# Kernel optimization log

Measured on AMD Instinct MI355X. Metric: run time of the kernel, lower is better.

## Reference

```python
import jax, jax.numpy as jnp
import numpy as np

N_NODES = 50000
N_EDGES = 600000
IN_FEATS = 128
N_HIDDEN = 128
N_CLASSES = 40


def setup_inputs() -> dict:
    key = jax.random.key(0)
    ks = jax.random.split(key, 12)
    feat = jax.random.normal(ks[0], (N_NODES, IN_FEATS), dtype=jnp.float32)
    src = jax.random.randint(ks[1], (N_EDGES,), 0, N_NODES, dtype=jnp.int32)
    dst = jax.random.randint(ks[2], (N_EDGES,), 0, N_NODES, dtype=jnp.int32)
    dims = [(IN_FEATS, N_HIDDEN), (N_HIDDEN, N_HIDDEN), (N_HIDDEN, N_CLASSES)]
    params = {}
    for i, (di, do) in enumerate(dims):
        s = 1.0 / np.sqrt(di)
        params[f"w_self{i}"] = jax.random.uniform(ks[3 + 3 * i], (di, do), jnp.float32, -s, s)
        params[f"w_neigh{i}"] = jax.random.uniform(ks[4 + 3 * i], (di, do), jnp.float32, -s, s)
        params[f"b{i}"] = jnp.zeros((do,), jnp.float32)
    return dict(feat=feat, src=src, dst=dst, **params)


def _sage_layer(h, src, dst, w_self, w_neigh, b):
    # mean aggregation over in-neighbors: msg = h[src], reduce at dst
    msg_sum = jax.ops.segment_sum(h[src], dst, num_segments=N_NODES)  # [N, d]
    deg = jax.ops.segment_sum(jnp.ones((src.shape[0],), h.dtype), dst, num_segments=N_NODES)
    h_neigh = msg_sum / jnp.maximum(deg, 1.0)[:, None]
    # DGL SAGEConv(mean): out = fc_self(h) + fc_neigh(mean_neigh) + bias
    return h @ w_self + h_neigh @ w_neigh + b


def reference(feat, src, dst,
              w_self0, w_neigh0, b0,
              w_self1, w_neigh1, b1,
              w_self2, w_neigh2, b2):
    # dropout p=0.0 -> identity
    h = _sage_layer(feat, src, dst, w_self0, w_neigh0, b0)
    h = jax.nn.relu(h)
    h = _sage_layer(h, src, dst, w_self1, w_neigh1, b1)
    h = jax.nn.relu(h)
    h = _sage_layer(h, src, dst, w_self2, w_neigh2, b2)
    return h
```

## Files before the change

### kernel.cpp

```cpp
#include <hip/hip_runtime.h>

#define N_NODES 50000
#define N_EDGES 600000

typedef short bf16x8 __attribute__((ext_vector_type(8)));
typedef float f32x4  __attribute__((ext_vector_type(4)));
typedef unsigned short u16x8 __attribute__((ext_vector_type(8)));
typedef unsigned short u16x4 __attribute__((ext_vector_type(4)));

__device__ inline ushort rne_bf16(float a) {
    union { float f; unsigned u; } v; v.f = a;
    return (ushort)((v.u + 0x7FFFu + ((v.u >> 16) & 1u)) >> 16);
}
__device__ inline float bf16_to_f32(ushort h) {
    return __uint_as_float((unsigned)h << 16);
}
__device__ inline void split_bf16(float a, ushort& hi, ushort& lo) {
    hi = rne_bf16(a);
    float hv = bf16_to_f32(hi);
    lo = rne_bf16(a - hv);
}


__global__ void count_deg_kernel(const int* __restrict__ dst, int* __restrict__ deg, int ne) {
    int e = blockIdx.x * blockDim.x + threadIdx.x;
    if (e < ne) atomicAdd(&deg[dst[e]], 1);
}

__global__ __launch_bounds__(256) void block_sums_kernel(const int* __restrict__ deg,
                                                         int* __restrict__ bsum, int n) {
    __shared__ int s[256];
    int t = threadIdx.x;
    int i = blockIdx.x * 256 + t;
    s[t] = (i < n) ? deg[i] : 0;
    __syncthreads();
    #pragma unroll
    for (int d = 128; d > 0; d >>= 1) {
        if (t < d) s[t] += s[t + d];
        __syncthreads();
    }
    if (t == 0) bsum[blockIdx.x] = s[0];
}

__global__ __launch_bounds__(256) void scatter_fused_kernel(const int* __restrict__ deg,
                                                            const int* __restrict__ bsum,
                                                            int* __restrict__ off,
                                                            int* __restrict__ cur,
                                                            int n, int nb) {
    __shared__ int s[256];
    int t = threadIdx.x;

    int bv = (t < nb) ? bsum[t] : 0;
    s[t] = bv;
    __syncthreads();
    #pragma unroll
    for (int d = 1; d < 256; d <<= 1) {
        int x = (t >= d) ? s[t - d] : 0;
        __syncthreads();
        s[t] += x;
        __syncthreads();
    }
    int base = (blockIdx.x > 0) ? s[blockIdx.x - 1] : 0;
    if (blockIdx.x == 0 && t == 0) off[n] = s[255];
    __syncthreads();

    int i = blockIdx.x * 256 + t;
    int v = (i < n) ? deg[i] : 0;
    s[t] = v;
    __syncthreads();
    #pragma unroll
    for (int d = 1; d < 256; d <<= 1) {
        int x = (t >= d) ? s[t - d] : 0;
        __syncthreads();
        s[t] += x;
        __syncthreads();
    }
    if (i < n) {
        int excl = s[t] - v + base;
        off[i] = excl;
        cur[i] = excl;
    }
}

__global__ void fill_csr_kernel(const int* __restrict__ src, const int* __restrict__ dst,
                                int* __restrict__ cur, int* __restrict__ ssrc, int ne) {
    int e = blockIdx.x * blockDim.x + threadIdx.x;
    if (e < ne) {
        int p = atomicAdd(&cur[dst[e]], 1);
        ssrc[p] = src[e];
    }
}

__global__ void convert_all_w(const float* __restrict__ ws0, const float* __restrict__ wn0,
                              const float* __restrict__ ws1, const float* __restrict__ wn1,
                              const float* __restrict__ ws2, const float* __restrict__ wn2,
                              ushort* __restrict__ Bth0, ushort* __restrict__ Btl0,
                              ushort* __restrict__ Bth1, ushort* __restrict__ Btl1,
                              ushort* __restrict__ Bth2, ushort* __restrict__ Btl2) {
    int b = blockIdx.x;
    int k = threadIdx.x;
    const float *Ws, *Wn;
    ushort *H, *L;
    int dout, n;
    if (b < 256)      { n = b;       dout = 128; Ws = ws0; Wn = wn0; H = Bth0; L = Btl0; }
    else if (b < 512) { n = b - 256; dout = 128; Ws = ws1; Wn = wn1; H = Bth1; L = Btl1; }
    else              { n = b - 512; dout = 40;  Ws = ws2; Wn = wn2; H = Bth2; L = Btl2; }
    float w = (n < dout) ? Ws[(long)k * dout + n] : Wn[(long)k * dout + (n - dout)];
    ushort hi, lo;
    split_bf16(w, hi, lo);
    H[n * 128 + k] = hi;
    L[n * 128 + k] = lo;
}


#define KDIM 128
#define APAD 136

__device__ inline void stage_a32(const float* __restrict__ A, int bm, int M, int tid,
                                 ushort* __restrict__ Ahi, ushort* __restrict__ Alo) {
    const int m   = tid >> 3;
    const int seg = (tid & 7) * 16;
    const int grow = bm + m;
    float f[16];
    if (grow < M) {
        const float* ap = A + (long)grow * KDIM + seg;
        #pragma unroll
        for (int q = 0; q < 4; ++q) {
            float4 a = *(const float4*)(ap + q * 4);
            f[q * 4 + 0] = a.x; f[q * 4 + 1] = a.y;
            f[q * 4 + 2] = a.z; f[q * 4 + 3] = a.w;
        }
    } else {
        #pragma unroll
        for (int i = 0; i < 16; ++i) f[i] = 0.f;
    }
    ushort h[16], l[16];
    #pragma unroll
    for (int i = 0; i < 16; ++i) split_bf16(f[i], h[i], l[i]);
    #pragma unroll
    for (int q = 0; q < 2; ++q) {
        uint4 hw, lw;
        hw.x = (unsigned)h[q*8+0] | ((unsigned)h[q*8+1] << 16);
        hw.y = (unsigned)h[q*8+2] | ((unsigned)h[q*8+3] << 16);
        hw.z = (unsigned)h[q*8+4] | ((unsigned)h[q*8+5] << 16);
        hw.w = (unsigned)h[q*8+6] | ((unsigned)h[q*8+7] << 16);
        lw.x = (unsigned)l[q*8+0] | ((unsigned)l[q*8+1] << 16);
        lw.y = (unsigned)l[q*8+2] | ((unsigned)l[q*8+3] << 16);
        lw.z = (unsigned)l[q*8+4] | ((unsigned)l[q*8+5] << 16);
        lw.w = (unsigned)l[q*8+6] | ((unsigned)l[q*8+7] << 16);
        *(uint4*)&Ahi[m * APAD + seg + q * 8] = hw;
        *(uint4*)&Alo[m * APAD + seg + q * 8] = lw;
    }
}

__global__ __launch_bounds__(256, 4) void gemm_mfma_wide(
    const float* __restrict__ A,
    const ushort* __restrict__ Bth, const ushort* __restrict__ Btl,
    const float* __restrict__ bias,
    float* __restrict__ S, ushort* __restrict__ T, int M)
{
    __shared__ ushort Ahi[32 * APAD];
    __shared__ ushort Alo[32 * APAD];

    const int tid = threadIdx.x;
    const int wave = tid >> 6;
    const int lane = tid & 63;
    const int lane16 = lane & 15;
    const int quad = lane >> 4;
    const int bm = blockIdx.x * 32;
    const int colbase = wave * 64;

    stage_a32(A, bm, M, tid, Ahi, Alo);
    __syncthreads();

    f32x4 acc[2][4] = {};

    #pragma unroll
    for (int c = 0; c < 4; ++c) {
        const int k0 = c * 32 + quad * 8;
        bf16x8 ah[2], al[2];
        #pragma unroll
        for (int r = 0; r < 2; ++r) {
            int off = (16 * r + lane16) * APAD + k0;
            ah[r] = *(const bf16x8*)&Ahi[off];
            al[r] = *(const bf16x8*)&Alo[off];
        }
        #pragma unroll
        for (int ct = 0; ct < 4; ++ct) {
            const long boff = (long)(colbase + 16 * ct + lane16) * KDIM + k0;
            bf16x8 bh = *(const bf16x8*)(Bth + boff);
            bf16x8 bl = *(const bf16x8*)(Btl + boff);
            #pragma unroll
            for (int r = 0; r < 2; ++r) {
                acc[r][ct] = __builtin_amdgcn_mfma_f32_16x16x32_bf16(bh, ah[r], acc[r][ct], 0, 0, 0);
                acc[r][ct] = __builtin_amdgcn_mfma_f32_16x16x32_bf16(bl, ah[r], acc[r][ct], 0, 0, 0);
                acc[r][ct] = __builtin_amdgcn_mfma_f32_16x16x32_bf16(bh, al[r], acc[r][ct], 0, 0, 0);
            }
        }
    }

    #pragma unroll
    for (int ct = 0; ct < 4; ++ct) {
        const int col0 = colbase + 16 * ct + quad * 4;
        const bool toS = col0 < 128;
        f32x4 bv = {0,0,0,0};
        if (toS) bv = *(const f32x4*)(bias + col0);
        #pragma unroll
        for (int r = 0; r < 2; ++r) {
            const int row = bm + 16 * r + lane16;
            if (row < M) {
                if (toS) {
                    *(f32x4*)(S + (long)row * 128 + col0) = acc[r][ct] + bv;
                } else {
                    u16x4 t4;
                    #pragma unroll
                    for (int i = 0; i < 4; ++i) t4[i] = rne_bf16(acc[r][ct][i]);
                    *(u16x4*)(T + (long)row * 128 + (col0 - 128)) = t4;
                }
            }
        }
    }
}

__global__ __launch_bounds__(256, 4) void gemm_mfma_narrow(
    const float* __restrict__ A,
    const ushort* __restrict__ Bth, const ushort* __restrict__ Btl,
    const float* __restrict__ bias,
    float* __restrict__ S, ushort* __restrict__ T, int M)
{
    __shared__ ushort Ahi[32 * APAD];
    __shared__ ushort Alo[32 * APAD];

    const int tid = threadIdx.x;
    const int wave = tid >> 6;
    const int lane = tid & 63;
    const int lane16 = lane & 15;
    const int quad = lane >> 4;
    const int bm = blockIdx.x * 32;

    const int rt = wave & 1;
    const int cg = wave >> 1;
    const int ctbase = cg * 3;
    const int nct = cg ? 2 : 3;

    stage_a32(A, bm, M, tid, Ahi, Alo);
    __syncthreads();

    f32x4 acc[3] = {};

    #pragma unroll
    for (int c = 0; c < 4; ++c) {
        const int off = (rt * 16 + lane16) * APAD + c * 32 + quad * 8;
        bf16x8 ah = *(const bf16x8*)&Ahi[off];
        bf16x8 al = *(const bf16x8*)&Alo[off];
        #pragma unroll
        for (int j = 0; j < 3; ++j) {
            if (j < nct) {
                const int ct = ctbase + j;
                const long boff = (long)(16 * ct + lane16) * KDIM + c * 32 + quad * 8;
                bf16x8 bh = *(const bf16x8*)(Bth + boff);
                bf16x8 bl = *(const bf16x8*)(Btl + boff);
                acc[j] = __builtin_amdgcn_mfma_f32_16x16x32_bf16(bh, ah, acc[j], 0, 0, 0);
                acc[j] = __builtin_amdgcn_mfma_f32_16x16x32_bf16(bl, ah, acc[j], 0, 0, 0);
                acc[j] = __builtin_amdgcn_mfma_f32_16x16x32_bf16(bh, al, acc[j], 0, 0, 0);
            }
        }
    }

    #pragma unroll
    for (int j = 0; j < 3; ++j) {
        if (j < nct) {
            const int ct = ctbase + j;
            const int col0 = 16 * ct + quad * 4;
            const bool toS = col0 < 40;
            const int row = bm + rt * 16 + lane16;
            if (row < M) {
                if (toS) {
                    f32x4 bv = *(const f32x4*)(bias + col0);
                    *(f32x4*)(S + (long)row * 40 + col0) = acc[j] + bv;
                } else {
                    u16x4 t4;
                    #pragma unroll
                    for (int i = 0; i < 4; ++i) t4[i] = rne_bf16(acc[j][i]);
                    *(u16x4*)(T + (long)row * 40 + (col0 - 40)) = t4;
                }
            }
        }
    }
}


template <int RELU>
__global__ __launch_bounds__(256) void agg128_kernel(
    const float* __restrict__ S, const ushort* __restrict__ T,
    const int* __restrict__ off, const int* __restrict__ ssrc,
    float* __restrict__ out, int nnodes)
{
    const int node = (blockIdx.x * 256 + threadIdx.x) >> 6;
    if (node >= nnodes) return;
    const int lane = threadIdx.x & 63;
    const int slot = lane >> 4;
    const int col8 = (lane & 15) * 8;

    const int a = off[node];
    const int b = off[node + 1];

    f32x4 acc0a = {0,0,0,0}, acc0b = {0,0,0,0};
    f32x4 acc1a = {0,0,0,0}, acc1b = {0,0,0,0};

    int i = a;
    for (; i + 8 <= b; i += 8) {
        int s0 = ssrc[i + slot];
        int s1 = ssrc[i + 4 + slot];
        u16x8 v0 = *(const u16x8*)(T + (long)s0 * 128 + col8);
        u16x8 v1 = *(const u16x8*)(T + (long)s1 * 128 + col8);
        #pragma unroll
        for (int j = 0; j < 4; ++j) {
            acc0a[j] += bf16_to_f32(v0[j]);
            acc0b[j] += bf16_to_f32(v0[4 + j]);
            acc1a[j] += bf16_to_f32(v1[j]);
            acc1b[j] += bf16_to_f32(v1[4 + j]);
        }
    }
    for (; i < b; i += 4) {
        int e = i + slot;
        if (e < b) {
            int s = ssrc[e];
            u16x8 v = *(const u16x8*)(T + (long)s * 128 + col8);
            #pragma unroll
            for (int j = 0; j < 4; ++j) {
                acc0a[j] += bf16_to_f32(v[j]);
                acc0b[j] += bf16_to_f32(v[4 + j]);
            }
        }
    }
    f32x4 accA = acc0a + acc1a;
    f32x4 accB = acc0b + acc1b;

    #pragma unroll
    for (int m = 16; m <= 32; m <<= 1) {
        #pragma unroll
        for (int j = 0; j < 4; ++j) {
            accA[j] += __shfl_xor((float)accA[j], m);
            accB[j] += __shfl_xor((float)accB[j], m);
        }
    }

    if (slot == 0) {
        int deg = b - a;
        float scale = (deg > 0) ? (1.0f / (float)deg) : 0.f;
        f32x4 sA = *(const f32x4*)(S + (long)node * 128 + col8);
        f32x4 sB = *(const f32x4*)(S + (long)node * 128 + col8 + 4);
        f32x4 rA = sA + accA * scale;
        f32x4 rB = sB + accB * scale;
        if (RELU) {
            #pragma unroll
            for (int j = 0; j < 4; ++j) {
                rA[j] = fmaxf(rA[j], 0.f);
                rB[j] = fmaxf(rB[j], 0.f);
            }
        }
        *(f32x4*)(out + (long)node * 128 + col8) = rA;
        *(f32x4*)(out + (long)node * 128 + col8 + 4) = rB;
    }
}

template <int RELU>
__global__ __launch_bounds__(256) void agg40_kernel(
    const float* __restrict__ S, const ushort* __restrict__ T,
    const int* __restrict__ off, const int* __restrict__ ssrc,
    float* __restrict__ out, int nnodes)
{
    const int node = (blockIdx.x * 256 + threadIdx.x) >> 6;
    if (node >= nnodes) return;
    const int lane = threadIdx.x & 63;
    const bool active = lane < 60;
    const int slot = active ? (lane / 10) : 5;
    const int fi = lane % 10;
    const int fo = fi * 4;

    const int a = off[node];
    const int b = off[node + 1];

    f32x4 acc0 = {0,0,0,0}, acc1 = {0,0,0,0};

    int i = a;
    for (; i + 12 <= b; i += 12) {
        int s0 = ssrc[i + slot];
        int s1 = ssrc[i + 6 + slot];
        u16x4 v0 = *(const u16x4*)(T + (long)s0 * 40 + fo);
        u16x4 v1 = *(const u16x4*)(T + (long)s1 * 40 + fo);
        if (active) {
            #pragma unroll
            for (int j = 0; j < 4; ++j) {
                acc0[j] += bf16_to_f32(v0[j]);
                acc1[j] += bf16_to_f32(v1[j]);
            }
        }
    }
    for (; i < b; i += 6) {
        int e = i + slot;
        if (active && e < b) {
            int s = ssrc[e];
            u16x4 v = *(const u16x4*)(T + (long)s * 40 + fo);
            #pragma unroll
            for (int j = 0; j < 4; ++j) acc0[j] += bf16_to_f32(v[j]);
        }
    }
    f32x4 acc = acc0 + acc1;

    f32x4 tot = acc;
    #pragma unroll
    for (int d = 10; d <= 50; d += 10) {
        int srcl = fi + d;
        #pragma unroll
        for (int j = 0; j < 4; ++j) tot[j] += __shfl((float)acc[j], srcl);
    }

    if (lane < 10) {
        int deg = b - a;
        float scale = (deg > 0) ? (1.0f / (float)deg) : 0.f;
        f32x4 s4 = *(const f32x4*)(S + (long)node * 40 + fo);
        f32x4 r = s4 + tot * scale;
        if (RELU) {
            #pragma unroll
            for (int j = 0; j < 4; ++j) r[j] = fmaxf(r[j], 0.f);
        }
        *(f32x4*)(out + (long)node * 40 + fo) = r;
    }
}


extern "C" void kernel_launch(void* const* d_in, const int* in_sizes, int n_in,
                              void* d_out, int out_size, void* d_ws, size_t ws_size,
                              hipStream_t stream) {
    const float* feat = (const float*)d_in[0];
    const int*   src  = (const int*)d_in[1];
    const int*   dst  = (const int*)d_in[2];
    const float* ws0  = (const float*)d_in[3];
    const float* wn0  = (const float*)d_in[4];
    const float* b0   = (const float*)d_in[5];
    const float* ws1  = (const float*)d_in[6];
    const float* wn1  = (const float*)d_in[7];
    const float* b1   = (const float*)d_in[8];
    const float* ws2  = (const float*)d_in[9];
    const float* wn2  = (const float*)d_in[10];
    const float* b2   = (const float*)d_in[11];

    const int N = N_NODES;
    const int NE = N_EDGES;
    const int NB = (N + 255) / 256;

    char* ws = (char*)d_ws;
    int*    offsets = (int*)(ws + 0);
    int*    cursor  = (int*)(ws + 200704);
    int*    degi    = (int*)(ws + 401408);
    int*    bsum    = (int*)(ws + 601600);
    int*    ssrc    = (int*)(ws + 603648);
    ushort* Bth0 = (ushort*)(ws + 200704);
    ushort* Btl0 = (ushort*)(ws + 266240);
    ushort* Bth1 = (ushort*)(ws + 331776);
    ushort* Btl1 = (ushort*)(ws + 397312);
    ushort* Bth2 = (ushort*)(ws + 462848);
    ushort* Btl2 = (ushort*)(ws + 483328);
    float*  hbuf = (float*)(ws + 3003904);
    float*  sbuf = (float*)(ws + 28603904);
    ushort* tbuf = (ushort*)(ws + 54203904);

    hipMemsetAsync(degi, 0, (size_t)N * sizeof(int), stream);
    count_deg_kernel<<<(NE + 255) / 256, 256, 0, stream>>>(dst, degi, NE);
    block_sums_kernel<<<NB, 256, 0, stream>>>(degi, bsum, N);
    scatter_fused_kernel<<<NB, 256, 0, stream>>>(degi, bsum, offsets, cursor, N, NB);
    fill_csr_kernel<<<(NE + 255) / 256, 256, 0, stream>>>(src, dst, cursor, ssrc, NE);

    convert_all_w<<<592, 128, 0, stream>>>(ws0, wn0, ws1, wn1, ws2, wn2,
                                           Bth0, Btl0, Bth1, Btl1, Bth2, Btl2);

    const int gx = (N + 31) / 32;
    const int ga = (N + 3) / 4;

    gemm_mfma_wide<<<gx, 256, 0, stream>>>(feat, Bth0, Btl0, b0, sbuf, tbuf, N);
    agg128_kernel<1><<<ga, 256, 0, stream>>>(sbuf, tbuf, offsets, ssrc, hbuf, N);

    gemm_mfma_wide<<<gx, 256, 0, stream>>>(hbuf, Bth1, Btl1, b1, sbuf, tbuf, N);
    agg128_kernel<1><<<ga, 256, 0, stream>>>(sbuf, tbuf, offsets, ssrc, hbuf, N);

    gemm_mfma_narrow<<<gx, 256, 0, stream>>>(hbuf, Bth2, Btl2, b2, sbuf, tbuf, N);
    agg40_kernel<0><<<ga, 256, 0, stream>>>(sbuf, tbuf, offsets, ssrc, (float*)d_out, N);
}
```

Before: 335.2 us.

## Split wide GEMM columns across block pairs with register-resident B fragments

Each wide-GEMM block now computes only one 128-column half (self or neighbor projection), preloading its B fragments into registers before a grid-stride loop over 32-row tiles. The grid is doubled so each block handles one tile. This halves per-block MFMA work and removes repeated B global loads inside the k-loop, at the cost of staging and splitting each A tile twice and a lower occupancy hint.

```diff
diff --git a/kernel.cpp b/kernel.cpp
--- a/kernel.cpp
+++ b/kernel.cpp
@@ -153,7 +153,7 @@
     }
 }
 
-__global__ __launch_bounds__(256, 4) void gemm_mfma_wide(
+__global__ __launch_bounds__(256, 3) void gemm_mfma_wide(
     const float* __restrict__ A,
     const ushort* __restrict__ Bth, const ushort* __restrict__ Btl,
     const float* __restrict__ bias,
@@ -167,55 +167,66 @@
     const int lane = tid & 63;
     const int lane16 = lane & 15;
     const int quad = lane >> 4;
-    const int bm = blockIdx.x * 32;
-    const int colbase = wave * 64;
-
-    stage_a32(A, bm, M, tid, Ahi, Alo);
-    __syncthreads();
-
-    f32x4 acc[2][4] = {};
-
+    const int half = blockIdx.x & 1;
+    const int colbase = half * 128 + wave * 32;
+    const int ntiles = (M + 31) >> 5;
+
+    bf16x8 Bh[4][2], Bl[4][2];
     #pragma unroll
     for (int c = 0; c < 4; ++c) {
-        const int k0 = c * 32 + quad * 8;
-        bf16x8 ah[2], al[2];
-        #pragma unroll
-        for (int r = 0; r < 2; ++r) {
-            int off = (16 * r + lane16) * APAD + k0;
-            ah[r] = *(const bf16x8*)&Ahi[off];
-            al[r] = *(const bf16x8*)&Alo[off];
-        }
-        #pragma unroll
-        for (int ct = 0; ct < 4; ++ct) {
-            const long boff = (long)(colbase + 16 * ct + lane16) * KDIM + k0;
-            bf16x8 bh = *(const bf16x8*)(Bth + boff);
-            bf16x8 bl = *(const bf16x8*)(Btl + boff);
+        #pragma unroll
+        for (int ct = 0; ct < 2; ++ct) {
+            const long boff = (long)(colbase + 16 * ct + lane16) * KDIM + c * 32 + quad * 8;
+            Bh[c][ct] = *(const bf16x8*)(Bth + boff);
+            Bl[c][ct] = *(const bf16x8*)(Btl + boff);
+        }
+    }
+
+    for (int rt = blockIdx.x >> 1; rt < ntiles; rt += gridDim.x >> 1) {
+        const int bm = rt * 32;
+        __syncthreads();
+        stage_a32(A, bm, M, tid, Ahi, Alo);
+        __syncthreads();
+
+        f32x4 acc[2][2] = {};
+
+        #pragma unroll
+        for (int c = 0; c < 4; ++c) {
+            const int k0 = c * 32 + quad * 8;
+            bf16x8 ah[2], al[2];
             #pragma unroll
             for (int r = 0; r < 2; ++r) {
-                acc[r][ct] = __builtin_amdgcn_mfma_f32_16x16x32_bf16(bh, ah[r], acc[r][ct], 0, 0, 0);
-                acc[r][ct] = __builtin_amdgcn_mfma_f32_16x16x32_bf16(bl, ah[r], acc[r][ct], 0, 0, 0);
-                acc[r][ct] = __builtin_amdgcn_mfma_f32_16x16x32_bf16(bh, al[r], acc[r][ct], 0, 0, 0);
-            }
-        }
-    }
-
-    #pragma unroll
-    for (int ct = 0; ct < 4; ++ct) {
-        const int col0 = colbase + 16 * ct + quad * 4;
-        const bool toS = col0 < 128;
-        f32x4 bv = {0,0,0,0};
-        if (toS) bv = *(const f32x4*)(bias + col0);
-        #pragma unroll
-        for (int r = 0; r < 2; ++r) {
-            const int row = bm + 16 * r + lane16;
-            if (row < M) {
-                if (toS) {
-                    *(f32x4*)(S + (long)row * 128 + col0) = acc[r][ct] + bv;
-                } else {
-                    u16x4 t4;
-                    #pragma unroll
-                    for (int i = 0; i < 4; ++i) t4[i] = rne_bf16(acc[r][ct][i]);
-                    *(u16x4*)(T + (long)row * 128 + (col0 - 128)) = t4;
+                int off = (16 * r + lane16) * APAD + k0;
+                ah[r] = *(const bf16x8*)&Ahi[off];
+                al[r] = *(const bf16x8*)&Alo[off];
+            }
+            #pragma unroll
+            for (int ct = 0; ct < 2; ++ct) {
+                #pragma unroll
+                for (int r = 0; r < 2; ++r) {
+                    acc[r][ct] = __builtin_amdgcn_mfma_f32_16x16x32_bf16(Bh[c][ct], ah[r], acc[r][ct], 0, 0, 0);
+                    acc[r][ct] = __builtin_amdgcn_mfma_f32_16x16x32_bf16(Bl[c][ct], ah[r], acc[r][ct], 0, 0, 0);
+                    acc[r][ct] = __builtin_amdgcn_mfma_f32_16x16x32_bf16(Bh[c][ct], al[r], acc[r][ct], 0, 0, 0);
+                }
+            }
+        }
+
+        #pragma unroll
+        for (int ct = 0; ct < 2; ++ct) {
+            const int colL = wave * 32 + 16 * ct + quad * 4;
+            #pragma unroll
+            for (int r = 0; r < 2; ++r) {
+                const int row = bm + 16 * r + lane16;
+                if (row < M) {
+                    if (half == 0) {
+                        f32x4 bv = *(const f32x4*)(bias + colL);
+                        *(f32x4*)(S + (long)row * 128 + colL) = acc[r][ct] + bv;
+                    } else {
+                        u16x4 t4;
+                        #pragma unroll
+                        for (int i = 0; i < 4; ++i) t4[i] = rne_bf16(acc[r][ct][i]);
+                        *(u16x4*)(T + (long)row * 128 + colL) = t4;
+                    }
                 }
             }
         }
@@ -476,15 +487,17 @@
     convert_all_w<<<592, 128, 0, stream>>>(ws0, wn0, ws1, wn1, ws2, wn2,
                                            Bth0, Btl0, Bth1, Btl1, Bth2, Btl2);
 
-    const int gx = (N + 31) / 32;
+    const int ntiles = (N + 31) / 32;
+    const int gw = 2 * ntiles;
+    const int gn = ntiles;
     const int ga = (N + 3) / 4;
 
-    gemm_mfma_wide<<<gx, 256, 0, stream>>>(feat, Bth0, Btl0, b0, sbuf, tbuf, N);
+    gemm_mfma_wide<<<gw, 256, 0, stream>>>(feat, Bth0, Btl0, b0, sbuf, tbuf, N);
     agg128_kernel<1><<<ga, 256, 0, stream>>>(sbuf, tbuf, offsets, ssrc, hbuf, N);
 
-    gemm_mfma_wide<<<gx, 256, 0, stream>>>(hbuf, Bth1, Btl1, b1, sbuf, tbuf, N);
+    gemm_mfma_wide<<<gw, 256, 0, stream>>>(hbuf, Bth1, Btl1, b1, sbuf, tbuf, N);
     agg128_kernel<1><<<ga, 256, 0, stream>>>(sbuf, tbuf, offsets, ssrc, hbuf, N);
 
-    gemm_mfma_narrow<<<gx, 256, 0, stream>>>(hbuf, Bth2, Btl2, b2, sbuf, tbuf, N);
+    gemm_mfma_narrow<<<gn, 256, 0, stream>>>(hbuf, Bth2, Btl2, b2, sbuf, tbuf, N);
     agg40_kernel<0><<<ga, 256, 0, stream>>>(sbuf, tbuf, offsets, ssrc, (float*)d_out, N);
 }
```

New measurement: 326.0 us. 2.7% less time.
